# Performance work log

Hardware: AMD Instinct MI355X
Metric: run time of the kernel (lower is better)

The kernel has to match this reference:

```python
import jax, jax.numpy as jnp
import numpy as np
import math

HEAD_DIM = 64
EMBED_DIM = 512
B, T = 16, 2048

def setup_inputs() -> dict:
    key = jax.random.key(0)
    k1, k2, k3 = jax.random.split(key, 3)
    x = jax.random.normal(k1, (B, T, EMBED_DIM), dtype=jnp.float32)
    # nn.Linear-style init scale
    s = 1.0 / math.sqrt(EMBED_DIM)
    Wq = jax.random.uniform(k2, (EMBED_DIM, HEAD_DIM), dtype=jnp.float32, minval=-s, maxval=s)
    bq = jax.random.uniform(k3, (HEAD_DIM,), dtype=jnp.float32, minval=-s, maxval=s)
    return {"x": x, "Wq": Wq, "bq": bq}

def reference(x, Wq, bq):
    # Faithful to source: q, k, v all come from the SAME query projection.
    q = jnp.einsum('bte,ed->btd', x, Wq) + bq  # [B,T,D]
    d_k = q.shape[-1]
    # weights[b, i, j] = q_i . q_j / sqrt(d_k)
    weights = jnp.einsum('bid,bjd->bij', q, q) / jnp.sqrt(jnp.float32(d_k))
    # NOTE: source applies softmax over dim=1 (query/row axis), not dim=-1.
    weights = jax.nn.softmax(weights, axis=1)
    attention = jnp.einsum('bij,bjd->bid', weights, q)  # v == q in source
    return attention
```

## Files before the change

### kernel.cpp

```cpp
#include <hip/hip_runtime.h>
#include <hip/hip_bf16.h>

#define BN 16
#define TN 2048
#define DN 64
#define EN 512
#define PAD 68

using f32x4  = __attribute__((ext_vector_type(4))) float;
using bf16x8 = __attribute__((ext_vector_type(8))) short;
using bf16x4 = __attribute__((ext_vector_type(4))) short;

static __device__ __forceinline__ short f2bf(float f) {
    __hip_bfloat16 h = __float2bfloat16(f);
    return __builtin_bit_cast(short, h);
}
static __device__ __forceinline__ float bf2f(short s) {
    return __bfloat162float(__builtin_bit_cast(__hip_bfloat16, s));
}
static __device__ __forceinline__ void bar_lds() {
    asm volatile("s_waitcnt lgkmcnt(0)" ::: "memory");
    __builtin_amdgcn_s_barrier();
}

__global__ __launch_bounds__(256) void wprep_kernel(
    const float* __restrict__ Wq, short* __restrict__ WTh,
    short* __restrict__ WTl)
{
    __shared__ float wlds[64][65];
    const int tid = threadIdx.x;
    const int k0 = blockIdx.x * 64;
    #pragma unroll
    for (int it = 0; it < 16; ++it) {
        int idx = it * 256 + tid;
        int k = idx >> 6, n = idx & 63;
        wlds[k][n] = Wq[(size_t)(k0 + k) * 64 + n];
    }
    __syncthreads();
    #pragma unroll
    for (int it = 0; it < 16; ++it) {
        int idx = it * 256 + tid;
        int n = idx >> 6, k = idx & 63;
        float v = wlds[k][n];
        short h = f2bf(v);
        short l = f2bf(v - bf2f(h));
        WTh[(size_t)n * EN + k0 + k] = h;
        WTl[(size_t)n * EN + k0 + k] = l;
    }
}

__global__ __launch_bounds__(256, 2) void qproj_kernel(
    const float* __restrict__ x, const short* __restrict__ WTh,
    const short* __restrict__ WTl, const float* __restrict__ bq,
    short* __restrict__ Qb, short* __restrict__ QTb)
{
    __shared__ short xh[2 * 64 * 40];
    __shared__ short wth[2 * 64 * 40];
    __shared__ short wtl[2 * 64 * 40];
    __shared__ short tl[64][68];

    const int tid = threadIdx.x;
    const int lane = tid & 63;
    const int wv = tid >> 6;
    const int c = lane & 15;
    const int g = lane >> 4;
    const int rowbase = blockIdx.x * 64;
    const int b = rowbase >> 11;
    const int tbase = rowbase & (TN - 1);

    const int sr = tid >> 3;
    const int sc4 = tid & 7;
    const size_t xr0 = (size_t)(rowbase + sr) * EN + sc4 * 4;
    const size_t xr1 = (size_t)(rowbase + 32 + sr) * EN + sc4 * 4;
    const size_t wr0 = (size_t)sr * EN + sc4 * 4;
    const size_t wr1 = (size_t)(32 + sr) * EN + sc4 * 4;

    float4 xa, xb;
    bf16x4 wa, wb, la, lb;

    xa = *reinterpret_cast<const float4*>(&x[xr0]);
    xb = *reinterpret_cast<const float4*>(&x[xr1]);
    wa = *reinterpret_cast<const bf16x4*>(&WTh[wr0]);
    wb = *reinterpret_cast<const bf16x4*>(&WTh[wr1]);
    la = *reinterpret_cast<const bf16x4*>(&WTl[wr0]);
    lb = *reinterpret_cast<const bf16x4*>(&WTl[wr1]);
    {
        bf16x4 h0, h1;
        #pragma unroll
        for (int j = 0; j < 4; ++j) { h0[j] = f2bf(xa[j]); h1[j] = f2bf(xb[j]); }
        *reinterpret_cast<bf16x4*>(&xh[sr * 40 + sc4 * 4]) = h0;
        *reinterpret_cast<bf16x4*>(&xh[(32 + sr) * 40 + sc4 * 4]) = h1;
        *reinterpret_cast<bf16x4*>(&wth[sr * 40 + sc4 * 4]) = wa;
        *reinterpret_cast<bf16x4*>(&wth[(32 + sr) * 40 + sc4 * 4]) = wb;
        *reinterpret_cast<bf16x4*>(&wtl[sr * 40 + sc4 * 4]) = la;
        *reinterpret_cast<bf16x4*>(&wtl[(32 + sr) * 40 + sc4 * 4]) = lb;
    }
    xa = *reinterpret_cast<const float4*>(&x[xr0 + 32]);
    xb = *reinterpret_cast<const float4*>(&x[xr1 + 32]);
    wa = *reinterpret_cast<const bf16x4*>(&WTh[wr0 + 32]);
    wb = *reinterpret_cast<const bf16x4*>(&WTh[wr1 + 32]);
    la = *reinterpret_cast<const bf16x4*>(&WTl[wr0 + 32]);
    lb = *reinterpret_cast<const bf16x4*>(&WTl[wr1 + 32]);
    bar_lds();

    f32x4 acc[4];
    #pragma unroll
    for (int nt = 0; nt < 4; ++nt) acc[nt] = (f32x4){0.f, 0.f, 0.f, 0.f};

    for (int t = 0; t < 16; ++t) {
        const int cur = t & 1;
        const int co = cur * 2560;
        if (t + 1 < 16) {
            const int wo = (cur ^ 1) * 2560;
            bf16x4 h0, h1;
            #pragma unroll
            for (int j = 0; j < 4; ++j) { h0[j] = f2bf(xa[j]); h1[j] = f2bf(xb[j]); }
            *reinterpret_cast<bf16x4*>(&xh[wo + sr * 40 + sc4 * 4]) = h0;
            *reinterpret_cast<bf16x4*>(&xh[wo + (32 + sr) * 40 + sc4 * 4]) = h1;
            *reinterpret_cast<bf16x4*>(&wth[wo + sr * 40 + sc4 * 4]) = wa;
            *reinterpret_cast<bf16x4*>(&wth[wo + (32 + sr) * 40 + sc4 * 4]) = wb;
            *reinterpret_cast<bf16x4*>(&wtl[wo + sr * 40 + sc4 * 4]) = la;
            *reinterpret_cast<bf16x4*>(&wtl[wo + (32 + sr) * 40 + sc4 * 4]) = lb;
        }
        if (t + 2 < 16) {
            const int kn = (t + 2) * 32;
            xa = *reinterpret_cast<const float4*>(&x[xr0 + kn]);
            xb = *reinterpret_cast<const float4*>(&x[xr1 + kn]);
            wa = *reinterpret_cast<const bf16x4*>(&WTh[wr0 + kn]);
            wb = *reinterpret_cast<const bf16x4*>(&WTh[wr1 + kn]);
            la = *reinterpret_cast<const bf16x4*>(&WTl[wr0 + kn]);
            lb = *reinterpret_cast<const bf16x4*>(&WTl[wr1 + kn]);
        }

        bf16x8 av = *reinterpret_cast<const bf16x8*>(&xh[co + (wv * 16 + c) * 40 + g * 8]);
        #pragma unroll
        for (int nt = 0; nt < 4; ++nt) {
            bf16x8 bh = *reinterpret_cast<const bf16x8*>(&wth[co + (nt * 16 + c) * 40 + g * 8]);
            bf16x8 bl = *reinterpret_cast<const bf16x8*>(&wtl[co + (nt * 16 + c) * 40 + g * 8]);
            acc[nt] = __builtin_amdgcn_mfma_f32_16x16x32_bf16(av, bh, acc[nt], 0, 0, 0);
            acc[nt] = __builtin_amdgcn_mfma_f32_16x16x32_bf16(av, bl, acc[nt], 0, 0, 0);
        }
        bar_lds();
    }

    __syncthreads();
    #pragma unroll
    for (int nt = 0; nt < 4; ++nt) {
        const float bias = bq[nt * 16 + c];
        #pragma unroll
        for (int r = 0; r < 4; ++r) {
            const int row = wv * 16 + g * 4 + r;
            short qb = f2bf(acc[nt][r] + bias);
            Qb[(size_t)(rowbase + row) * DN + nt * 16 + c] = qb;
            tl[nt * 16 + c][row] = qb;
        }
    }
    __syncthreads();
    #pragma unroll
    for (int it = 0; it < 4; ++it) {
        int idx = it * 256 + tid;
        int d = idx >> 4;
        int j4 = (idx & 15) * 4;
        *reinterpret_cast<short4*>(&QTb[((size_t)(b * 64 + d)) * TN + tbase + j4]) =
            *reinterpret_cast<const short4*>(&tl[d][j4]);
    }
}

__global__ __launch_bounds__(256, 4) void stats_kernel(
    const short* __restrict__ Qb, float* __restrict__ l_part)
{
    __shared__ short Qt[2 * 64 * PAD];
    const int tid = threadIdx.x;
    const int lane = tid & 63;
    const int wv = tid >> 6;
    const int c = lane & 15;
    const int g = lane >> 4;
    const int b = blockIdx.y;
    const int z = blockIdx.z;
    const int jbase = blockIdx.x * 64 + wv * 16;
    const short* Qbb = Qb + (size_t)b * TN * DN;

    bf16x8 a0 = *reinterpret_cast<const bf16x8*>(Qbb + (size_t)(jbase + c) * DN + g * 8);
    bf16x8 a1 = *reinterpret_cast<const bf16x8*>(Qbb + (size_t)(jbase + c) * DN + g * 8 + 32);

    const int srow = tid >> 2;
    const int schk = tid & 3;
    const int ilo = z * (TN / 4);
    const int NT = (TN / 4) / 64;

    bf16x8 v0, v1;
    v0 = *reinterpret_cast<const bf16x8*>(Qbb + (size_t)(ilo + srow) * DN + schk * 16);
    v1 = *reinterpret_cast<const bf16x8*>(Qbb + (size_t)(ilo + srow) * DN + schk * 16 + 8);
    *reinterpret_cast<bf16x8*>(&Qt[srow * PAD + schk * 16]) = v0;
    *reinterpret_cast<bf16x8*>(&Qt[srow * PAD + schk * 16 + 8]) = v1;
    v0 = *reinterpret_cast<const bf16x8*>(Qbb + (size_t)(ilo + 64 + srow) * DN + schk * 16);
    v1 = *reinterpret_cast<const bf16x8*>(Qbb + (size_t)(ilo + 64 + srow) * DN + schk * 16 + 8);
    bar_lds();

    float l[4] = {0.f, 0.f, 0.f, 0.f};
    for (int t = 0; t < NT; ++t) {
        const int cur = t & 1;
        const int co = cur * 64 * PAD;
        if (t + 1 < NT) {
            const int wo = (cur ^ 1) * 64 * PAD;
            *reinterpret_cast<bf16x8*>(&Qt[wo + srow * PAD + schk * 16]) = v0;
            *reinterpret_cast<bf16x8*>(&Qt[wo + srow * PAD + schk * 16 + 8]) = v1;
        }
        if (t + 2 < NT) {
            const int in_ = ilo + (t + 2) * 64;
            v0 = *reinterpret_cast<const bf16x8*>(Qbb + (size_t)(in_ + srow) * DN + schk * 16);
            v1 = *reinterpret_cast<const bf16x8*>(Qbb + (size_t)(in_ + srow) * DN + schk * 16 + 8);
        }
        #pragma unroll
        for (int it = 0; it < 4; ++it) {
            bf16x8 b0 = *reinterpret_cast<const bf16x8*>(&Qt[co + (it * 16 + c) * PAD + g * 8]);
            bf16x8 b1 = *reinterpret_cast<const bf16x8*>(&Qt[co + (it * 16 + c) * PAD + g * 8 + 32]);
            f32x4 acc = {0.f, 0.f, 0.f, 0.f};
            acc = __builtin_amdgcn_mfma_f32_16x16x32_bf16(a0, b0, acc, 0, 0, 0);
            acc = __builtin_amdgcn_mfma_f32_16x16x32_bf16(a1, b1, acc, 0, 0, 0);
            #pragma unroll
            for (int r = 0; r < 4; ++r)
                l[r] += __expf(acc[r] * 0.125f);
        }
        bar_lds();
    }
    #pragma unroll
    for (int r = 0; r < 4; ++r) {
        float v = l[r];
        v += __shfl_xor(v, 1);
        v += __shfl_xor(v, 2);
        v += __shfl_xor(v, 4);
        v += __shfl_xor(v, 8);
        l[r] = v;
    }
    if (c == 0) {
        #pragma unroll
        for (int r = 0; r < 4; ++r)
            l_part[((size_t)z * BN + b) * TN + jbase + g * 4 + r] = l[r];
    }
}

__global__ __launch_bounds__(256) void fuse_kernel(
    const short* __restrict__ QTb, const float* __restrict__ l_part,
    short* __restrict__ RT)
{
    const int idx = blockIdx.x * 256 + threadIdx.x;
    const int c8 = idx & 255;
    const int bd = idx >> 8;
    const int b = bd >> 6;
    const int j0 = c8 * 8;

    bf16x8 q = *reinterpret_cast<const bf16x8*>(&QTb[(size_t)bd * TN + j0]);
    const float* lp0 = l_part + (size_t)b * TN + j0;
    const float* lp1 = l_part + (size_t)(BN + b) * TN + j0;
    const float* lp2 = l_part + (size_t)(2 * BN + b) * TN + j0;
    const float* lp3 = l_part + (size_t)(3 * BN + b) * TN + j0;
    bf16x8 r;
    #pragma unroll
    for (int t = 0; t < 8; ++t)
        r[t] = f2bf(bf2f(q[t]) / (lp0[t] + lp1[t] + lp2[t] + lp3[t]));
    *reinterpret_cast<bf16x8*>(&RT[(size_t)bd * TN + j0]) = r;
}

__global__ __launch_bounds__(256, 2) void pv_kernel(
    const short* __restrict__ Qb, const short* __restrict__ RT,
    float* __restrict__ out0, float* __restrict__ out1)
{
    __shared__ short Qt[2 * 64 * PAD];
    __shared__ short RTt[2 * 64 * PAD];
    __shared__ short Pt[8][16 * PAD];

    const int tid = threadIdx.x;
    const int lane = tid & 63;
    const int wv = tid >> 6;
    const int c = lane & 15;
    const int g = lane >> 4;
    const int b = blockIdx.y;
    const int z = blockIdx.z;
    const int ibase = blockIdx.x * 128 + wv * 32;
    const short* Qbb = Qb + (size_t)b * TN * DN;
    const short* RTb = RT + (size_t)b * DN * TN;

    bf16x8 bi[2][2];
    #pragma unroll
    for (int ih = 0; ih < 2; ++ih) {
        const short* p = Qbb + (size_t)(ibase + ih * 16 + c) * DN + g * 8;
        bi[ih][0] = *reinterpret_cast<const bf16x8*>(p);
        bi[ih][1] = *reinterpret_cast<const bf16x8*>(p + 32);
    }

    f32x4 o[4][2];
    #pragma unroll
    for (int dt = 0; dt < 4; ++dt)
        #pragma unroll
        for (int ih = 0; ih < 2; ++ih)
            o[dt][ih] = (f32x4){0.f, 0.f, 0.f, 0.f};

    const int srow = tid >> 2;
    const int schk = tid & 3;
    const int jlo = z * (TN / 2);
    const int NT = (TN / 2) / 64;

    bf16x8 vq0, vq1, vt0, vt1;
    vq0 = *reinterpret_cast<const bf16x8*>(Qbb + (size_t)(jlo + srow) * DN + schk * 16);
    vq1 = *reinterpret_cast<const bf16x8*>(Qbb + (size_t)(jlo + srow) * DN + schk * 16 + 8);
    vt0 = *reinterpret_cast<const bf16x8*>(RTb + (size_t)srow * TN + jlo + schk * 16);
    vt1 = *reinterpret_cast<const bf16x8*>(RTb + (size_t)srow * TN + jlo + schk * 16 + 8);
    *reinterpret_cast<bf16x8*>(&Qt[srow * PAD + schk * 16]) = vq0;
    *reinterpret_cast<bf16x8*>(&Qt[srow * PAD + schk * 16 + 8]) = vq1;
    *reinterpret_cast<bf16x8*>(&RTt[srow * PAD + schk * 16]) = vt0;
    *reinterpret_cast<bf16x8*>(&RTt[srow * PAD + schk * 16 + 8]) = vt1;
    vq0 = *reinterpret_cast<const bf16x8*>(Qbb + (size_t)(jlo + 64 + srow) * DN + schk * 16);
    vq1 = *reinterpret_cast<const bf16x8*>(Qbb + (size_t)(jlo + 64 + srow) * DN + schk * 16 + 8);
    vt0 = *reinterpret_cast<const bf16x8*>(RTb + (size_t)srow * TN + jlo + 64 + schk * 16);
    vt1 = *reinterpret_cast<const bf16x8*>(RTb + (size_t)srow * TN + jlo + 64 + schk * 16 + 8);
    bar_lds();

    for (int t = 0; t < NT; ++t) {
        const int cur = t & 1;
        const int co = cur * 64 * PAD;
        if (t + 1 < NT) {
            const int wo = (cur ^ 1) * 64 * PAD;
            *reinterpret_cast<bf16x8*>(&Qt[wo + srow * PAD + schk * 16]) = vq0;
            *reinterpret_cast<bf16x8*>(&Qt[wo + srow * PAD + schk * 16 + 8]) = vq1;
            *reinterpret_cast<bf16x8*>(&RTt[wo + srow * PAD + schk * 16]) = vt0;
            *reinterpret_cast<bf16x8*>(&RTt[wo + srow * PAD + schk * 16 + 8]) = vt1;
        }
        if (t + 2 < NT) {
            const int jn = jlo + (t + 2) * 64;
            vq0 = *reinterpret_cast<const bf16x8*>(Qbb + (size_t)(jn + srow) * DN + schk * 16);
            vq1 = *reinterpret_cast<const bf16x8*>(Qbb + (size_t)(jn + srow) * DN + schk * 16 + 8);
            vt0 = *reinterpret_cast<const bf16x8*>(RTb + (size_t)srow * TN + jn + schk * 16);
            vt1 = *reinterpret_cast<const bf16x8*>(RTb + (size_t)srow * TN + jn + schk * 16 + 8);
        }

        bf16x8 aq[4][2];
        #pragma unroll
        for (int dt = 0; dt < 4; ++dt) {
            aq[dt][0] = *reinterpret_cast<const bf16x8*>(&RTt[co + (dt * 16 + c) * PAD + g * 8]);
            aq[dt][1] = *reinterpret_cast<const bf16x8*>(&RTt[co + (dt * 16 + c) * PAD + 32 + g * 8]);
        }

        #pragma unroll
        for (int jt = 0; jt < 4; ++jt) {
            bf16x8 a0 = *reinterpret_cast<const bf16x8*>(&Qt[co + (jt * 16 + c) * PAD + g * 8]);
            bf16x8 a1 = *reinterpret_cast<const bf16x8*>(&Qt[co + (jt * 16 + c) * PAD + g * 8 + 32]);
            #pragma unroll
            for (int ih = 0; ih < 2; ++ih) {
                f32x4 accs = {0.f, 0.f, 0.f, 0.f};
                accs = __builtin_amdgcn_mfma_f32_16x16x32_bf16(a0, bi[ih][0], accs, 0, 0, 0);
                accs = __builtin_amdgcn_mfma_f32_16x16x32_bf16(a1, bi[ih][1], accs, 0, 0, 0);
                bf16x4 pw;
                #pragma unroll
                for (int r = 0; r < 4; ++r)
                    pw[r] = f2bf(__expf(accs[r] * 0.125f));
                *reinterpret_cast<bf16x4*>(&Pt[wv * 2 + ih][c * PAD + jt * 16 + g * 4]) = pw;
            }
        }
        asm volatile("s_waitcnt lgkmcnt(0)" ::: "memory");
        __builtin_amdgcn_sched_barrier(0);

        #pragma unroll
        for (int ih = 0; ih < 2; ++ih) {
            bf16x8 p0 = *reinterpret_cast<const bf16x8*>(&Pt[wv * 2 + ih][c * PAD + g * 8]);
            bf16x8 p1 = *reinterpret_cast<const bf16x8*>(&Pt[wv * 2 + ih][c * PAD + 32 + g * 8]);
            #pragma unroll
            for (int dt = 0; dt < 4; ++dt) {
                o[dt][ih] = __builtin_amdgcn_mfma_f32_16x16x32_bf16(aq[dt][0], p0, o[dt][ih], 0, 0, 0);
                o[dt][ih] = __builtin_amdgcn_mfma_f32_16x16x32_bf16(aq[dt][1], p1, o[dt][ih], 0, 0, 0);
            }
        }
        bar_lds();
    }

    float* outb = (z ? out1 : out0) + (size_t)b * TN * DN;
    #pragma unroll
    for (int dt = 0; dt < 4; ++dt) {
        #pragma unroll
        for (int ih = 0; ih < 2; ++ih) {
            float4 v4;
            v4.x = o[dt][ih][0]; v4.y = o[dt][ih][1];
            v4.z = o[dt][ih][2]; v4.w = o[dt][ih][3];
            *reinterpret_cast<float4*>(
                &outb[(size_t)(ibase + ih * 16 + c) * DN + dt * 16 + g * 4]) = v4;
        }
    }
}

__global__ __launch_bounds__(256) void reduce_kernel(
    float* __restrict__ out, const float* __restrict__ part1)
{
    const size_t i = (size_t)blockIdx.x * 256 + threadIdx.x;
    float4 a = reinterpret_cast<float4*>(out)[i];
    float4 b = reinterpret_cast<const float4*>(part1)[i];
    a.x += b.x; a.y += b.y; a.z += b.z; a.w += b.w;
    reinterpret_cast<float4*>(out)[i] = a;
}

extern "C" void kernel_launch(void* const* d_in, const int* in_sizes, int n_in,
                              void* d_out, int out_size, void* d_ws, size_t ws_size,
                              hipStream_t stream) {
    const float* x  = (const float*)d_in[0];
    const float* Wq = (const float*)d_in[1];
    const float* bq = (const float*)d_in[2];
    float* out = (float*)d_out;

    short* Qb   = (short*)d_ws;
    short* QTb  = Qb + (size_t)BN * TN * DN;
    short* RT   = QTb + (size_t)BN * TN * DN;
    float* lpar = (float*)(RT + (size_t)BN * TN * DN);
    short* WTh  = (short*)(lpar + (size_t)4 * BN * TN);
    short* WTl  = WTh + (size_t)DN * EN;
    float* part1 = (float*)(WTl + (size_t)DN * EN);

    wprep_kernel<<<dim3(EN / 64), dim3(256), 0, stream>>>(Wq, WTh, WTl);
    qproj_kernel<<<dim3(BN * TN / 64), dim3(256), 0, stream>>>(x, WTh, WTl, bq, Qb, QTb);
    stats_kernel<<<dim3(TN / 64, BN, 4), dim3(256), 0, stream>>>(Qb, lpar);
    fuse_kernel<<<dim3(BN * DN * TN / 8 / 256), dim3(256), 0, stream>>>(QTb, lpar, RT);
    pv_kernel<<<dim3(TN / 128, BN, 2), dim3(256), 0, stream>>>(Qb, RT, out, part1);
    reduce_kernel<<<dim3(BN * TN * DN / 4 / 256), dim3(256), 0, stream>>>(out, part1);
}
```

Before: 78.75 us.

## Fold softmax normalization into PV kernel and pre-scale Q for exp2

Drops the separate fuse kernel that wrote a normalized transposed Q (RT). The PV kernel now loads the unscaled transposed Q directly and applies the reciprocal column sums while forming the probability tile. Separately, the bf16 Q used for scores is pre-scaled by sqrt(log2(e)/sqrt(d)), so both the stats and PV kernels can call exp2 without a per-element multiply. This removes one launch and the read and write of a 4 MB intermediate. It adds a small per-tile load of the four partial sums plus a reciprocal in PV, and changes bf16 rounding slightly.

Result: slower. 88.00 us (+11.7%).

```diff
diff --git a/kernel.cpp b/kernel.cpp
--- a/kernel.cpp
+++ b/kernel.cpp
@@ -6,6 +6,7 @@
 #define DN 64
 #define EN 512
 #define PAD 68
+#define SQK 0.42466084f
 
 using f32x4  = __attribute__((ext_vector_type(4))) float;
 using bf16x8 = __attribute__((ext_vector_type(8))) short;
@@ -150,9 +151,9 @@
         #pragma unroll
         for (int r = 0; r < 4; ++r) {
             const int row = wv * 16 + g * 4 + r;
-            short qb = f2bf(acc[nt][r] + bias);
-            Qb[(size_t)(rowbase + row) * DN + nt * 16 + c] = qb;
-            tl[nt * 16 + c][row] = qb;
+            const float q = acc[nt][r] + bias;
+            Qb[(size_t)(rowbase + row) * DN + nt * 16 + c] = f2bf(q * SQK);
+            tl[nt * 16 + c][row] = f2bf(q);
         }
     }
     __syncthreads();
@@ -220,7 +221,7 @@
             acc = __builtin_amdgcn_mfma_f32_16x16x32_bf16(a1, b1, acc, 0, 0, 0);
             #pragma unroll
             for (int r = 0; r < 4; ++r)
-                l[r] += __expf(acc[r] * 0.125f);
+                l[r] += __builtin_exp2f(acc[r]);
         }
         bar_lds();
     }
@@ -240,35 +241,15 @@
     }
 }
 
-__global__ __launch_bounds__(256) void fuse_kernel(
-    const short* __restrict__ QTb, const float* __restrict__ l_part,
-    short* __restrict__ RT)
-{
-    const int idx = blockIdx.x * 256 + threadIdx.x;
-    const int c8 = idx & 255;
-    const int bd = idx >> 8;
-    const int b = bd >> 6;
-    const int j0 = c8 * 8;
-
-    bf16x8 q = *reinterpret_cast<const bf16x8*>(&QTb[(size_t)bd * TN + j0]);
-    const float* lp0 = l_part + (size_t)b * TN + j0;
-    const float* lp1 = l_part + (size_t)(BN + b) * TN + j0;
-    const float* lp2 = l_part + (size_t)(2 * BN + b) * TN + j0;
-    const float* lp3 = l_part + (size_t)(3 * BN + b) * TN + j0;
-    bf16x8 r;
-    #pragma unroll
-    for (int t = 0; t < 8; ++t)
-        r[t] = f2bf(bf2f(q[t]) / (lp0[t] + lp1[t] + lp2[t] + lp3[t]));
-    *reinterpret_cast<bf16x8*>(&RT[(size_t)bd * TN + j0]) = r;
-}
-
 __global__ __launch_bounds__(256, 2) void pv_kernel(
-    const short* __restrict__ Qb, const short* __restrict__ RT,
+    const short* __restrict__ Qb, const short* __restrict__ QTb,
+    const float* __restrict__ l_part,
     float* __restrict__ out0, float* __restrict__ out1)
 {
     __shared__ short Qt[2 * 64 * PAD];
-    __shared__ short RTt[2 * 64 * PAD];
+    __shared__ short QTt[2 * 64 * PAD];
     __shared__ short Pt[8][16 * PAD];
+    __shared__ float lv[2][64];
 
     const int tid = threadIdx.x;
     const int lane = tid & 63;
@@ -279,7 +260,11 @@
     const int z = blockIdx.z;
     const int ibase = blockIdx.x * 128 + wv * 32;
     const short* Qbb = Qb + (size_t)b * TN * DN;
-    const short* RTb = RT + (size_t)b * DN * TN;
+    const short* QTbb = QTb + (size_t)b * DN * TN;
+    const float* lp0 = l_part + (size_t)b * TN;
+    const float* lp1 = l_part + (size_t)(BN + b) * TN;
+    const float* lp2 = l_part + (size_t)(2 * BN + b) * TN;
+    const float* lp3 = l_part + (size_t)(3 * BN + b) * TN;
 
     bf16x8 bi[2][2];
     #pragma unroll
@@ -302,18 +287,27 @@
     const int NT = (TN / 2) / 64;
 
     bf16x8 vq0, vq1, vt0, vt1;
+    float vl = 0.f;
     vq0 = *reinterpret_cast<const bf16x8*>(Qbb + (size_t)(jlo + srow) * DN + schk * 16);
     vq1 = *reinterpret_cast<const bf16x8*>(Qbb + (size_t)(jlo + srow) * DN + schk * 16 + 8);
-    vt0 = *reinterpret_cast<const bf16x8*>(RTb + (size_t)srow * TN + jlo + schk * 16);
-    vt1 = *reinterpret_cast<const bf16x8*>(RTb + (size_t)srow * TN + jlo + schk * 16 + 8);
+    vt0 = *reinterpret_cast<const bf16x8*>(QTbb + (size_t)srow * TN + jlo + schk * 16);
+    vt1 = *reinterpret_cast<const bf16x8*>(QTbb + (size_t)srow * TN + jlo + schk * 16 + 8);
     *reinterpret_cast<bf16x8*>(&Qt[srow * PAD + schk * 16]) = vq0;
     *reinterpret_cast<bf16x8*>(&Qt[srow * PAD + schk * 16 + 8]) = vq1;
-    *reinterpret_cast<bf16x8*>(&RTt[srow * PAD + schk * 16]) = vt0;
-    *reinterpret_cast<bf16x8*>(&RTt[srow * PAD + schk * 16 + 8]) = vt1;
+    *reinterpret_cast<bf16x8*>(&QTt[srow * PAD + schk * 16]) = vt0;
+    *reinterpret_cast<bf16x8*>(&QTt[srow * PAD + schk * 16 + 8]) = vt1;
+    if (tid < 64) {
+        const int j = jlo + tid;
+        lv[0][tid] = 1.0f / (lp0[j] + lp1[j] + lp2[j] + lp3[j]);
+    }
     vq0 = *reinterpret_cast<const bf16x8*>(Qbb + (size_t)(jlo + 64 + srow) * DN + schk * 16);
     vq1 = *reinterpret_cast<const bf16x8*>(Qbb + (size_t)(jlo + 64 + srow) * DN + schk * 16 + 8);
-    vt0 = *reinterpret_cast<const bf16x8*>(RTb + (size_t)srow * TN + jlo + 64 + schk * 16);
-    vt1 = *reinterpret_cast<const bf16x8*>(RTb + (size_t)srow * TN + jlo + 64 + schk * 16 + 8);
+    vt0 = *reinterpret_cast<const bf16x8*>(QTbb + (size_t)srow * TN + jlo + 64 + schk * 16);
+    vt1 = *reinterpret_cast<const bf16x8*>(QTbb + (size_t)srow * TN + jlo + 64 + schk * 16 + 8);
+    if (tid < 64) {
+        const int j = jlo + 64 + tid;
+        vl = 1.0f / (lp0[j] + lp1[j] + lp2[j] + lp3[j]);
+    }
     bar_lds();
 
     for (int t = 0; t < NT; ++t) {
@@ -323,28 +317,34 @@
             const int wo = (cur ^ 1) * 64 * PAD;
             *reinterpret_cast<bf16x8*>(&Qt[wo + srow * PAD + schk * 16]) = vq0;
             *reinterpret_cast<bf16x8*>(&Qt[wo + srow * PAD + schk * 16 + 8]) = vq1;
-            *reinterpret_cast<bf16x8*>(&RTt[wo + srow * PAD + schk * 16]) = vt0;
-            *reinterpret_cast<bf16x8*>(&RTt[wo + srow * PAD + schk * 16 + 8]) = vt1;
+            *reinterpret_cast<bf16x8*>(&QTt[wo + srow * PAD + schk * 16]) = vt0;
+            *reinterpret_cast<bf16x8*>(&QTt[wo + srow * PAD + schk * 16 + 8]) = vt1;
+            if (tid < 64) lv[cur ^ 1][tid] = vl;
         }
         if (t + 2 < NT) {
             const int jn = jlo + (t + 2) * 64;
             vq0 = *reinterpret_cast<const bf16x8*>(Qbb + (size_t)(jn + srow) * DN + schk * 16);
             vq1 = *reinterpret_cast<const bf16x8*>(Qbb + (size_t)(jn + srow) * DN + schk * 16 + 8);
-            vt0 = *reinterpret_cast<const bf16x8*>(RTb + (size_t)srow * TN + jn + schk * 16);
-            vt1 = *reinterpret_cast<const bf16x8*>(RTb + (size_t)srow * TN + jn + schk * 16 + 8);
+            vt0 = *reinterpret_cast<const bf16x8*>(QTbb + (size_t)srow * TN + jn + schk * 16);
+            vt1 = *reinterpret_cast<const bf16x8*>(QTbb + (size_t)srow * TN + jn + schk * 16 + 8);
+            if (tid < 64) {
+                const int j = jn + tid;
+                vl = 1.0f / (lp0[j] + lp1[j] + lp2[j] + lp3[j]);
+            }
         }
 
         bf16x8 aq[4][2];
         #pragma unroll
         for (int dt = 0; dt < 4; ++dt) {
-            aq[dt][0] = *reinterpret_cast<const bf16x8*>(&RTt[co + (dt * 16 + c) * PAD + g * 8]);
-            aq[dt][1] = *reinterpret_cast<const bf16x8*>(&RTt[co + (dt * 16 + c) * PAD + 32 + g * 8]);
+            aq[dt][0] = *reinterpret_cast<const bf16x8*>(&QTt[co + (dt * 16 + c) * PAD + g * 8]);
+            aq[dt][1] = *reinterpret_cast<const bf16x8*>(&QTt[co + (dt * 16 + c) * PAD + 32 + g * 8]);
         }
 
         #pragma unroll
         for (int jt = 0; jt < 4; ++jt) {
             bf16x8 a0 = *reinterpret_cast<const bf16x8*>(&Qt[co + (jt * 16 + c) * PAD + g * 8]);
             bf16x8 a1 = *reinterpret_cast<const bf16x8*>(&Qt[co + (jt * 16 + c) * PAD + g * 8 + 32]);
+            f32x4 lw = *reinterpret_cast<const f32x4*>(&lv[cur][jt * 16 + g * 4]);
             #pragma unroll
             for (int ih = 0; ih < 2; ++ih) {
                 f32x4 accs = {0.f, 0.f, 0.f, 0.f};
@@ -353,7 +353,7 @@
                 bf16x4 pw;
                 #pragma unroll
                 for (int r = 0; r < 4; ++r)
-                    pw[r] = f2bf(__expf(accs[r] * 0.125f));
+                    pw[r] = f2bf(__builtin_exp2f(accs[r]) * lw[r]);
                 *reinterpret_cast<bf16x4*>(&Pt[wv * 2 + ih][c * PAD + jt * 16 + g * 4]) = pw;
             }
         }
@@ -407,8 +407,7 @@
 
     short* Qb   = (short*)d_ws;
     short* QTb  = Qb + (size_t)BN * TN * DN;
-    short* RT   = QTb + (size_t)BN * TN * DN;
-    float* lpar = (float*)(RT + (size_t)BN * TN * DN);
+    float* lpar = (float*)(QTb + (size_t)BN * TN * DN);
     short* WTh  = (short*)(lpar + (size_t)4 * BN * TN);
     short* WTl  = WTh + (size_t)DN * EN;
     float* part1 = (float*)(WTl + (size_t)DN * EN);
@@ -416,7 +415,6 @@
     wprep_kernel<<<dim3(EN / 64), dim3(256), 0, stream>>>(Wq, WTh, WTl);
     qproj_kernel<<<dim3(BN * TN / 64), dim3(256), 0, stream>>>(x, WTh, WTl, bq, Qb, QTb);
     stats_kernel<<<dim3(TN / 64, BN, 4), dim3(256), 0, stream>>>(Qb, lpar);
-    fuse_kernel<<<dim3(BN * DN * TN / 8 / 256), dim3(256), 0, stream>>>(QTb, lpar, RT);
-    pv_kernel<<<dim3(TN / 128, BN, 2), dim3(256), 0, stream>>>(Qb, RT, out, part1);
+    pv_kernel<<<dim3(TN / 128, BN, 2), dim3(256), 0, stream>>>(Qb, QTb, lpar, out, part1);
     reduce_kernel<<<dim3(BN * TN * DN / 4 / 256), dim3(256), 0, stream>>>(out, part1);
 }
```
